# Kernel tuning notes

Measured on AMD Instinct MI355X. Metric: run time of the kernel, lower is better.

## Reference

```python
import jax, jax.numpy as jnp
import numpy as np

N, D, H, DPE, WALK, L, E = 2048, 512, 8, 16, 8, 3, 32768
HD = D // H
DFF = 4 * D


def setup_inputs() -> dict:
    key = jax.random.key(0)
    ks = jax.random.split(key, 16)
    s = 0.02
    return {
        "node_features": jax.random.normal(ks[0], (N, D), jnp.float32),
        "edge_index": jax.random.randint(ks[1], (2, E), 0, N, dtype=jnp.int32),
        "pe_proj_W": jax.random.normal(ks[2], (WALK, DPE), jnp.float32) * s,
        "pe_proj_b": jnp.zeros((DPE,), jnp.float32),
        "qkv_W": jax.random.normal(ks[3], (L, D, 3 * D), jnp.float32) * s,
        "qkv_b": jnp.zeros((L, 3 * D), jnp.float32),
        "peb_W": jax.random.normal(ks[4], (L, DPE, H), jnp.float32) * s,
        "peb_b": jnp.zeros((L, H), jnp.float32),
        "out_W": jax.random.normal(ks[5], (L, D, D), jnp.float32) * s,
        "out_b": jnp.zeros((L, D), jnp.float32),
        "ffn_W1": jax.random.normal(ks[6], (L, D, DFF), jnp.float32) * s,
        "ffn_b1": jnp.zeros((L, DFF), jnp.float32),
        "ffn_W2": jax.random.normal(ks[7], (L, DFF, D), jnp.float32) * s,
        "ffn_b2": jnp.zeros((L, D), jnp.float32),
        "ln1_g": jnp.ones((L, D), jnp.float32),
        "ln1_b": jnp.zeros((L, D), jnp.float32),
        "ln2_g": jnp.ones((L, D), jnp.float32),
        "ln2_b": jnp.zeros((L, D), jnp.float32),
    }


def _layer_norm(x, g, b, eps=1e-5):
    mu = x.mean(-1, keepdims=True)
    var = ((x - mu) ** 2).mean(-1, keepdims=True)
    return (x - mu) * jax.lax.rsqrt(var + eps) * g + b


def _rw_pe(edge_index, pe_proj_W, pe_proj_b, dtype):
    src, tgt = edge_index[0], edge_index[1]
    adj = jnp.zeros((N, N), dtype).at[src, tgt].set(1.0).at[tgt, src].set(1.0)
    deg = jnp.maximum(adj.sum(axis=1, keepdims=True), 1.0)
    T = adj / deg  # row-stochastic transition matrix

    def step(Tk, _):
        return Tk @ T, jnp.diagonal(Tk)

    _, diags = jax.lax.scan(step, T, None, length=WALK)  # [WALK, N]
    rw = diags.T  # [N, WALK] k-step return probabilities
    return rw @ pe_proj_W + pe_proj_b  # [N, DPE]


def reference(node_features, edge_index, pe_proj_W, pe_proj_b, qkv_W, qkv_b,
              peb_W, peb_b, out_W, out_b, ffn_W1, ffn_b1, ffn_W2, ffn_b2,
              ln1_g, ln1_b, ln2_g, ln2_b):
    pe = _rw_pe(edge_index, pe_proj_W, pe_proj_b, node_features.dtype)
    scale = HD ** -0.5
    x = node_features
    for l in range(L):
        qkv = (x @ qkv_W[l] + qkv_b[l]).reshape(N, 3, H, HD)
        q = jnp.transpose(qkv[:, 0], (1, 0, 2))  # [H, N, HD]
        k = jnp.transpose(qkv[:, 1], (1, 0, 2))
        v = jnp.transpose(qkv[:, 2], (1, 0, 2))
        pe_p = pe @ peb_W[l] + peb_b[l]  # [N, H]
        # bias[h, i, j] = pe_p[i, h] - pe_p[j, h]
        bias = pe_p.T[:, :, None] - pe_p.T[:, None, :]
        scores = jnp.einsum('hnd,hmd->hnm', q, k) * scale + bias
        attn = jax.nn.softmax(scores, axis=-1)
        o = jnp.einsum('hnm,hmd->hnd', attn, v)
        o = jnp.transpose(o, (1, 0, 2)).reshape(N, D) @ out_W[l] + out_b[l]
        x = _layer_norm(x + o, ln1_g[l], ln1_b[l])
        h = jax.nn.gelu(x @ ffn_W1[l] + ffn_b1[l], approximate=False)
        h = h @ ffn_W2[l] + ffn_b2[l]
        x = _layer_norm(x + h, ln2_g[l], ln2_b[l])
    return x
```

## Files before the change

### kernel.cpp

```cpp
#include <hip/hip_runtime.h>
#include <cstdint>
#include <cstddef>

#define NN 2048
#define DM 512
#define NH 8
#define HD 64
#define NL 3
#define DFFV 2048
#define NE 32768

typedef unsigned short u16;
typedef unsigned int u32;
typedef __attribute__((ext_vector_type(8))) short short8;
typedef __attribute__((ext_vector_type(4))) float float4v;

__device__ __forceinline__ float bf2f(u16 s){
  union { unsigned u; float f; } v; v.u = ((unsigned)s) << 16; return v.f;
}
__device__ __forceinline__ u16 f2bf(float f){
  union { float f; unsigned u; } v; v.f = f;
  unsigned r = v.u + 0x7fffu + ((v.u >> 16) & 1u);
  return (u16)(r >> 16);
}
__device__ __forceinline__ u16 f2bf_fast(float f){
  union { float f; unsigned u; } v; v.f = f;
  return (u16)((v.u + 0x8000u) >> 16);
}
__device__ __forceinline__ void gl_lds16(const void* g, void* l){
  __builtin_amdgcn_global_load_lds((const __attribute__((address_space(1))) void*)g,
                                   (__attribute__((address_space(3))) void*)l, 16, 0, 0);
}

__global__ void adj_scatter(const int* __restrict__ ei, float* __restrict__ A){
  int e = blockIdx.x*256 + threadIdx.x;
  if (e < NE){
    int s = ei[e], t = ei[NE + e];
    A[(size_t)s*NN + t] = 1.f;
    A[(size_t)t*NN + s] = 1.f;
  }
}

__global__ __launch_bounds__(256)
void rowsum_dinv(const float* __restrict__ A, float* __restrict__ dinv){
  int row = blockIdx.x, tid = threadIdx.x;
  __shared__ float red[4];
  float s = 0.f;
  for (int j=tid;j<NN;j+=256) s += A[(size_t)row*NN + j];
  #pragma unroll
  for (int off=32;off>0;off>>=1) s += __shfl_down(s, off);
  if ((tid&63)==0) red[tid>>6] = s;
  __syncthreads();
  if (tid==0) dinv[row] = rsqrtf(fmaxf(red[0]+red[1]+red[2]+red[3], 1.f));
}

__global__ void build_s(const float* __restrict__ A, const float* __restrict__ dinv,
                        u16* __restrict__ S){
  int j = blockIdx.x*256 + threadIdx.x;
  int i = blockIdx.y;
  float a = A[(size_t)i*NN + j];
  S[(size_t)i*NN + j] = f2bf(a * dinv[i] * dinv[j]);
}

__global__ __launch_bounds__(256)
void extract_nz(const u16* __restrict__ S, u32* __restrict__ nz, int* __restrict__ cnt){
  const int j = blockIdx.x, tid = threadIdx.x;
  __shared__ int lc;
  if (tid==0) lc = 0;
  __syncthreads();
  for (int c=tid; c<NN; c+=256){
    u16 v = S[(size_t)j*NN + c];
    if (v){
      int s = atomicAdd(&lc, 1);
      if (s < 128) nz[j*128 + s] = ((u32)c << 16) | v;
    }
  }
  __syncthreads();
  if (tid==0) cnt[j] = lc < 128 ? lc : 128;
}

__global__ __launch_bounds__(256)
void spmm(const u16* __restrict__ Bold, const u32* __restrict__ nz,
          const int* __restrict__ cnt, u16* __restrict__ Bnew)
{
  const int j = blockIdx.x, tid = threadIdx.x;
  __shared__ u32 lnz[128];
  __shared__ int lcnt;
  if (tid==0) lcnt = cnt[j];
  if (tid<128) lnz[tid] = nz[j*128 + tid];
  __syncthreads();
  const int n = lcnt;
  float acc[8] = {0,0,0,0,0,0,0,0};
  for (int e=0; e<n; e++){
    u32 p = lnz[e];
    int k = p >> 16;
    float wv = bf2f((u16)(p & 0xffffu));
    short8 rv = *(const short8*)&Bold[(size_t)k*NN + tid*8];
    #pragma unroll
    for (int t=0;t<8;t++) acc[t] = fmaf(bf2f((u16)rv[t]), wv, acc[t]);
  }
  short8 o;
  #pragma unroll
  for (int t=0;t<8;t++) o[t] = (short)f2bf(acc[t]);
  *(short8*)&Bnew[(size_t)j*NN + tid*8] = o;
}

__global__ __launch_bounds__(256)
void diag_pe(const u16* __restrict__ S, const u16* __restrict__ S2,
             const u16* __restrict__ S3, const u16* __restrict__ S4,
             const float* __restrict__ peW, const float* __restrict__ peb,
             float* __restrict__ pe)
{
  const int i = blockIdx.x, tid = threadIdx.x;
  float d[7] = {0,0,0,0,0,0,0};
  for (int j=tid;j<NN;j+=256){
    float s1 = bf2f(S [(size_t)i*NN + j]);
    float s2 = bf2f(S2[(size_t)i*NN + j]);
    float s3 = bf2f(S3[(size_t)i*NN + j]);
    float s4 = bf2f(S4[(size_t)i*NN + j]);
    d[0] += s1*s1; d[1] += s1*s2; d[2] += s2*s2; d[3] += s2*s3;
    d[4] += s3*s3; d[5] += s3*s4; d[6] += s4*s4;
  }
  __shared__ float red[28];
  #pragma unroll
  for (int t=0;t<7;t++){
    float v = d[t];
    #pragma unroll
    for (int off=32;off>0;off>>=1) v += __shfl_down(v, off);
    if ((tid&63)==0) red[t*4 + (tid>>6)] = v;
  }
  __syncthreads();
  if (tid < 16){
    float rr[8];
    rr[0] = bf2f(S[(size_t)i*NN + i]);
    #pragma unroll
    for (int t=0;t<7;t++) rr[t+1] = red[t*4]+red[t*4+1]+red[t*4+2]+red[t*4+3];
    float a = peb[tid];
    #pragma unroll
    for (int k=0;k<8;k++) a += rr[k]*peW[k*16 + tid];
    pe[(size_t)i*16 + tid] = a;
  }
}

__global__ void pe_proj2(const float* __restrict__ pe, const float* __restrict__ pebW,
                         const float* __restrict__ pebb, float* __restrict__ pebT){
  int n = blockIdx.x*256 + threadIdx.x;
  float pv[16];
  #pragma unroll
  for (int p=0;p<16;p++) pv[p] = pe[(size_t)n*16+p];
  for (int l=0;l<NL;l++)
    for (int h=0;h<NH;h++){
      float a = pebb[l*NH+h];
      #pragma unroll
      for (int p=0;p<16;p++) a += pv[p]*pebW[(l*16+p)*NH+h];
      pebT[((size_t)l*NH+h)*NN + n] = a;
    }
}

__global__ void init_x(const float* __restrict__ nf, float* __restrict__ x, u16* __restrict__ xbf){
  size_t i = (size_t)blockIdx.x*256 + threadIdx.x;
  float v = nf[i]; x[i] = v; xbf[i] = f2bf(v);
}

__global__ void transpose_w(const float* __restrict__ W, u16* __restrict__ WT, int K, int N){
  __shared__ float t[32][33];
  int l = blockIdx.z;
  W  += (size_t)l*K*N;
  WT += (size_t)l*K*N;
  int n0 = blockIdx.x*32, k0 = blockIdx.y*32;
  int tx = threadIdx.x, ty = threadIdx.y;
  #pragma unroll
  for (int i=0;i<32;i+=8) t[ty+i][tx] = W[(size_t)(k0+ty+i)*N + n0+tx];
  __syncthreads();
  #pragma unroll
  for (int i=0;i<32;i+=8) WT[(size_t)(n0+ty+i)*K + k0+tx] = f2bf(t[tx][ty+i]);
}

__global__ void pack_vt(const u16* __restrict__ qkv, u16* __restrict__ vT){
  __shared__ u16 t[32][33];
  int h = blockIdx.z, n0 = blockIdx.x*32, d0 = blockIdx.y*32;
  int tx = threadIdx.x, ty = threadIdx.y;
  #pragma unroll
  for (int i=0;i<32;i+=8) t[ty+i][tx] = qkv[(size_t)(n0+ty+i)*1536 + 1024 + h*64 + d0+tx];
  __syncthreads();
  #pragma unroll
  for (int i=0;i<32;i+=8) vT[(size_t)(h*64 + d0+ty+i)*NN + n0+tx] = t[tx][ty+i];
}

__global__ __launch_bounds__(256)
void ln_kernel(const float* __restrict__ xin, const float* __restrict__ add, int nsl,
               const float* __restrict__ g, const float* __restrict__ b,
               float* __restrict__ xout, u16* __restrict__ xbf)
{
  const int row = blockIdx.x, tid = threadIdx.x;
  __shared__ float red[8];
  const size_t base = (size_t)row*DM;
  float v0 = xin[base+tid];
  float v1 = xin[base+256+tid];
  for (int s=0;s<nsl;s++){
    v0 += add[(size_t)s*NN*DM + base+tid];
    v1 += add[(size_t)s*NN*DM + base+256+tid];
  }
  float s = v0+v1, sq = v0*v0 + v1*v1;
  #pragma unroll
  for (int off=32; off>0; off>>=1){ s += __shfl_down(s, off); sq += __shfl_down(sq, off); }
  if ((tid&63)==0){ red[tid>>6] = s; red[4+(tid>>6)] = sq; }
  __syncthreads();
  float mean = (red[0]+red[1]+red[2]+red[3]) * (1.f/512.f);
  float var  = (red[4]+red[5]+red[6]+red[7]) * (1.f/512.f) - mean*mean;
  float rstd = rsqrtf(var + 1e-5f);
  float y0 = (v0-mean)*rstd*g[tid]     + b[tid];
  float y1 = (v1-mean)*rstd*g[256+tid] + b[256+tid];
  xout[base+tid] = y0;     xout[base+256+tid] = y1;
  xbf[base+tid]  = f2bf(y0); xbf[base+256+tid] = f2bf(y1);
}

template<int OUTMODE, int GELU, int BIAS>
__global__ __launch_bounds__(256)
void gemm64(const u16* __restrict__ A, const u16* __restrict__ BT,
            const float* __restrict__ bias, void* __restrict__ Cout,
            int M, int N, int K, int ldc, int kper)
{
  __shared__ u16 As[64*32];
  __shared__ u16 Bs[64*32];
  const int tid = threadIdx.x, lane = tid & 63, wave = tid >> 6;
  const int q = lane >> 4, lo = lane & 15;
  const int bm = blockIdx.y, bn = blockIdx.x;
  const int wm = wave >> 1, wn = wave & 1;
  const int k_begin = blockIdx.z * kper, k_end = k_begin + kper;
  const int lrow  = lane >> 2;
  const int lkoff = (lane & 3) * 8;

  const u16* Ag = A  + ((size_t)bm*64 + 16*wave + lrow) * (size_t)K;
  const u16* Bg = BT + ((size_t)bn*64 + 16*wave + lrow) * (size_t)K;
  u16* AsW = As + (16*wave)*32;
  u16* BsW = Bs + (16*wave)*32;

  float4v acc[2][2] = {};

  for (int k0 = k_begin; k0 < k_end; k0 += 32){
    __syncthreads();
    gl_lds16(Ag + k0 + lkoff, AsW);
    gl_lds16(Bg + k0 + lkoff, BsW);
    __syncthreads();
    const short8* Ar = (const short8*)As;
    const short8* Br = (const short8*)Bs;
    short8 af[2], bfr[2];
    #pragma unroll
    for (int mt=0;mt<2;mt++) af[mt]  = Ar[(32*wm + 16*mt + lo)*4 + q];
    #pragma unroll
    for (int nt=0;nt<2;nt++) bfr[nt] = Br[(32*wn + 16*nt + lo)*4 + q];
    #pragma unroll
    for (int mt=0;mt<2;mt++)
      #pragma unroll
      for (int nt=0;nt<2;nt++)
        acc[mt][nt] = __builtin_amdgcn_mfma_f32_16x16x32_bf16(af[mt], bfr[nt], acc[mt][nt], 0, 0, 0);
  }

  float* Cf = (float*)Cout;
  u16*   Cb = (u16*)Cout;
  const size_t zoff = (OUTMODE == 2) ? (size_t)blockIdx.z * M * ldc : 0;
  #pragma unroll
  for (int mt=0;mt<2;mt++){
    const int row = bm*64 + 32*wm + 16*mt + q*4;
    #pragma unroll
    for (int nt=0;nt<2;nt++){
      const int col = bn*64 + 32*wn + 16*nt + lo;
      float bb = BIAS ? bias[col] : 0.f;
      #pragma unroll
      for (int r=0;r<4;r++){
        float v = acc[mt][nt][r];
        if (OUTMODE == 2){
          if (BIAS && blockIdx.z == 0) v += bb;
          Cf[zoff + (size_t)(row+r)*ldc + col] = v;
        } else {
          v += bb;
          if (GELU) v = 0.5f*v*(1.f + erff(v*0.70710678118654752f));
          if (OUTMODE == 1) Cb[(size_t)(row+r)*ldc + col] = f2bf(v);
          else              Cf[(size_t)(row+r)*ldc + col] = v;
        }
      }
    }
  }
}

__global__ __launch_bounds__(256)
void attn_part(const u16* __restrict__ qkv, const u16* __restrict__ vT,
               const float* __restrict__ pebT, float* __restrict__ Opart,
               float* __restrict__ Lsum)
{
  __shared__ u16 Ks[64*72];
  __shared__ u16 Vs[64*72];
  __shared__ u16 Ps[64*72];
  __shared__ float CB[64];
  const int tid = threadIdx.x, lane = tid&63, wave = tid>>6;
  const int q = lane>>4, lo = lane&15;
  const int qb = blockIdx.x, h = blockIdx.y, ks = blockIdx.z;
  const int i0 = qb*64;
  const int part = (ks*NH + h)*32 + qb;

  short8 qf[2];
  #pragma unroll
  for (int kk=0;kk<2;kk++)
    qf[kk] = *(const short8*)&qkv[(size_t)(i0 + 16*wave + lo)*1536 + h*64 + kk*32 + q*8];

  float l_r[4] = {0.f,0.f,0.f,0.f};
  float4v o_acc[4] = {};

  const int j_begin = ks*512, j_end = j_begin + 512;
  for (int j0 = j_begin; j0 < j_end; j0 += 64){
    __syncthreads();
    for (int c = tid; c < 512; c += 256){
      int row = c >> 3, off = c & 7;
      *(float4v*)&Ks[row*72 + off*8] =
        *(const float4v*)&qkv[(size_t)(j0+row)*1536 + 512 + h*64 + off*8];
      *(float4v*)&Vs[row*72 + off*8] =
        *(const float4v*)&vT[(size_t)(h*64+row)*NN + j0 + off*8];
    }
    if (tid < 64) CB[tid] = pebT[(size_t)h*NN + j0 + tid] * 1.4426950408889634f;
    __syncthreads();

    float4v sacc[4] = {};
    const short8* Kr = (const short8*)Ks;
    #pragma unroll
    for (int kk=0; kk<2; kk++){
      #pragma unroll
      for (int nt=0; nt<4; nt++){
        short8 bfr = Kr[(16*nt + lo)*9 + kk*4 + q];
        sacc[nt] = __builtin_amdgcn_mfma_f32_16x16x32_bf16(qf[kk], bfr, sacc[nt], 0,0,0);
      }
    }
    #pragma unroll
    for (int nt=0; nt<4; nt++){
      float cb = CB[16*nt + lo];
      #pragma unroll
      for (int r=0;r<4;r++){
        float p = exp2f(fmaf(sacc[nt][r], 0.180336880f, -cb));
        l_r[r] += p;
        Ps[(16*wave + q*4 + r)*72 + 16*nt + lo] = f2bf_fast(p);
      }
    }
    const short8* Pr = (const short8*)Ps;
    const short8* Vr = (const short8*)Vs;
    #pragma unroll
    for (int kk=0;kk<2;kk++){
      short8 af = Pr[(16*wave + lo)*9 + kk*4 + q];
      #pragma unroll
      for (int nt=0;nt<4;nt++){
        short8 bfr = Vr[(16*nt + lo)*9 + kk*4 + q];
        o_acc[nt] = __builtin_amdgcn_mfma_f32_16x16x32_bf16(af, bfr, o_acc[nt], 0,0,0);
      }
    }
  }
  #pragma unroll
  for (int r=0;r<4;r++){
    float s = l_r[r];
    s += __shfl_xor(s, 1);
    s += __shfl_xor(s, 2);
    s += __shfl_xor(s, 4);
    s += __shfl_xor(s, 8);
    l_r[r] = s;
  }
  float* Op = Opart + (size_t)part*4096;
  #pragma unroll
  for (int nt=0;nt<4;nt++){
    #pragma unroll
    for (int r=0;r<4;r++)
      Op[(16*wave + q*4 + r)*64 + 16*nt + lo] = o_acc[nt][r];
  }
  if (lo == 0){
    #pragma unroll
    for (int r=0;r<4;r++)
      Lsum[part*64 + 16*wave + q*4 + r] = l_r[r];
  }
}

__global__ __launch_bounds__(256)
void attn_combine(const float* __restrict__ Opart, const float* __restrict__ Lsum,
                  u16* __restrict__ obuf)
{
  const int qb = blockIdx.x, h = blockIdx.y, tid = threadIdx.x;
  __shared__ float invL[64];
  if (tid < 64){
    float L = 0.f;
    #pragma unroll
    for (int k=0;k<4;k++) L += Lsum[((k*NH + h)*32 + qb)*64 + tid];
    invL[tid] = 1.f / L;
  }
  __syncthreads();
  const int col = tid & 63, r0 = (tid >> 6) * 16;
  #pragma unroll
  for (int r=0;r<16;r++){
    int row = r0 + r;
    float acc = 0.f;
    #pragma unroll
    for (int k=0;k<4;k++)
      acc += Opart[((size_t)((k*NH + h)*32 + qb))*4096 + row*64 + col];
    obuf[(size_t)(qb*64 + row)*DM + h*64 + col] = f2bf(acc * invL[row]);
  }
}

extern "C" void kernel_launch(void* const* d_in, const int* in_sizes, int n_in,
                              void* d_out, int out_size, void* d_ws, size_t ws_size,
                              hipStream_t stream) {
  const float* nf   = (const float*)d_in[0];
  const int*   ei   = (const int*)d_in[1];
  const float* peW  = (const float*)d_in[2];
  const float* peb  = (const float*)d_in[3];
  const float* qkvW = (const float*)d_in[4];
  const float* qkvb = (const float*)d_in[5];
  const float* pebW = (const float*)d_in[6];
  const float* pebb = (const float*)d_in[7];
  const float* outW = (const float*)d_in[8];
  const float* outb = (const float*)d_in[9];
  const float* f1W  = (const float*)d_in[10];
  const float* f1b  = (const float*)d_in[11];
  const float* f2W  = (const float*)d_in[12];
  const float* f2b  = (const float*)d_in[13];
  const float* ln1g = (const float*)d_in[14];
  const float* ln1b = (const float*)d_in[15];
  const float* ln2g = (const float*)d_in[16];
  const float* ln2b = (const float*)d_in[17];
  (void)in_sizes; (void)n_in; (void)out_size; (void)ws_size;

  char* w = (char*)d_ws;
  constexpr size_t OFF_A     = 0;
  constexpr size_t OFF_S     = OFF_A + 16777216;
  constexpr size_t OFF_S2    = OFF_S + 8388608;
  constexpr size_t OFF_S3    = OFF_S2 + 8388608;
  constexpr size_t OFF_S4    = OFF_S3 + 8388608;
  constexpr size_t OFF_DINV  = OFF_S4 + 8388608;
  constexpr size_t OFF_PE    = OFF_DINV + 8192;
  constexpr size_t OFF_PEBT  = OFF_PE + 131072;
  constexpr size_t OFF_QKVT  = OFF_PEBT + 196608;
  constexpr size_t OFF_OUTT  = OFF_QKVT + 4718592;
  constexpr size_t OFF_F1T   = OFF_OUTT + 1572864;
  constexpr size_t OFF_F2T   = OFF_F1T + 6291456;
  constexpr size_t OFF_X     = OFF_F2T + 6291456;
  constexpr size_t OFF_XBF   = OFF_X + 4194304;
  constexpr size_t OFF_QKVB  = OFF_XBF + 2097152;
  constexpr size_t OFF_VT    = OFF_QKVB + 6291456;
  constexpr size_t OFF_OBUF  = OFF_VT + 2097152;
  constexpr size_t OFF_NZ    = OFF_OBUF + 2097152;
  constexpr size_t OFF_CNT   = OFF_NZ + 1048576;
  constexpr size_t OFF_ML    = OFF_CNT + 8192;
  constexpr size_t OFF_HBUF  = OFF_ML + 524288;

  float* A     = (float*)(w + OFF_A);
  u16*   S     = (u16*)  (w + OFF_S);
  u16*   S2    = (u16*)  (w + OFF_S2);
  u16*   S3    = (u16*)  (w + OFF_S3);
  u16*   S4    = (u16*)  (w + OFF_S4);
  float* dinv  = (float*)(w + OFF_DINV);
  float* pe    = (float*)(w + OFF_PE);
  float* pebT  = (float*)(w + OFF_PEBT);
  u16*   qkvT  = (u16*)  (w + OFF_QKVT);
  u16*   outT  = (u16*)  (w + OFF_OUTT);
  u16*   f1T   = (u16*)  (w + OFF_F1T);
  u16*   f2T   = (u16*)  (w + OFF_F2T);
  float* x     = (float*)(w + OFF_X);
  u16*   xbf   = (u16*)  (w + OFF_XBF);
  u16*   qkvB  = (u16*)  (w + OFF_QKVB);
  u16*   vT    = (u16*)  (w + OFF_VT);
  u16*   obuf  = (u16*)  (w + OFF_OBUF);
  u32*   NZ    = (u32*)  (w + OFF_NZ);
  int*   CNT   = (int*)  (w + OFF_CNT);
  float* Lsum  = (float*)(w + OFF_ML);
  u16*   hbuf  = (u16*)  (w + OFF_HBUF);
  float* Opart = A;

  hipMemsetAsync(A, 0, 16777216, stream);
  adj_scatter<<<dim3(NE/256), 256, 0, stream>>>(ei, A);
  rowsum_dinv<<<dim3(NN), 256, 0, stream>>>(A, dinv);
  build_s<<<dim3(NN/256, NN), 256, 0, stream>>>(A, dinv, S);
  extract_nz<<<dim3(NN), 256, 0, stream>>>(S, NZ, CNT);
  spmm<<<dim3(NN), 256, 0, stream>>>(S,  NZ, CNT, S2);
  spmm<<<dim3(NN), 256, 0, stream>>>(S2, NZ, CNT, S3);
  spmm<<<dim3(NN), 256, 0, stream>>>(S3, NZ, CNT, S4);
  diag_pe<<<dim3(NN), 256, 0, stream>>>(S, S2, S3, S4, peW, peb, pe);
  pe_proj2<<<dim3(NN/256), 256, 0, stream>>>(pe, pebW, pebb, pebT);

  transpose_w<<<dim3(1536/32, 512/32, NL), dim3(32,8), 0, stream>>>(qkvW, qkvT, 512, 1536);
  transpose_w<<<dim3(512/32,  512/32, NL), dim3(32,8), 0, stream>>>(outW, outT, 512, 512);
  transpose_w<<<dim3(2048/32, 512/32, NL), dim3(32,8), 0, stream>>>(f1W,  f1T,  512, 2048);
  transpose_w<<<dim3(512/32, 2048/32, NL), dim3(32,8), 0, stream>>>(f2W,  f2T,  2048, 512);
  init_x<<<dim3(NN*DM/256), 256, 0, stream>>>(nf, x, xbf);

  for (int l = 0; l < NL; l++){
    gemm64<1,0,1><<<dim3(24,32,1), 256, 0, stream>>>(
        xbf, qkvT + (size_t)l*1536*512, qkvb + l*1536, qkvB, 2048, 1536, 512, 1536, 512);
    pack_vt<<<dim3(64,2,8), dim3(32,8), 0, stream>>>(qkvB, vT);
    attn_part<<<dim3(32,8,4), 256, 0, stream>>>(qkvB, vT, pebT + (size_t)l*NH*NN, Opart, Lsum);
    attn_combine<<<dim3(32,8), 256, 0, stream>>>(Opart, Lsum, obuf);

    gemm64<2,0,1><<<dim3(8,32,2), 256, 0, stream>>>(
        obuf, outT + (size_t)l*512*512, outb + l*512, A, 2048, 512, 512, 512, 256);
    ln_kernel<<<dim3(NN), 256, 0, stream>>>(x, A, 2, ln1g + l*512, ln1b + l*512, x, xbf);

    gemm64<1,1,1><<<dim3(32,32,1), 256, 0, stream>>>(
        xbf, f1T + (size_t)l*2048*512, f1b + l*2048, hbuf, 2048, 2048, 512, 2048, 512);
    gemm64<2,0,1><<<dim3(8,32,4), 256, 0, stream>>>(
        hbuf, f2T + (size_t)l*512*2048, f2b + l*512, A, 2048, 512, 2048, 512, 512);
    ln_kernel<<<dim3(NN), 256, 0, stream>>>(x, A, 4, ln2g + l*512, ln2b + l*512, x, xbf);
  }

  hipMemcpyAsync(d_out, x, (size_t)NN*DM*4, hipMemcpyDeviceToDevice, stream);
}
```

Baseline: 513.4 us.

## Fuse preprocessing kernels, compute V transposed via GEMM, enlarge attention query tiles

Merges build_s with nonzero extraction, folds the per-layer PE bias projection into diag_pe, and merges the four weight transposes into one launch. This cuts launch count and extra passes over the 2048x2048 matrices. V^T is now produced directly by a swapped-operand GEMM with a row-bias mode, which removes the pack_vt kernel. Attention processes 128 query rows per block so each K/V tile is reused more. The final layer norm writes straight to the output, which removes the trailing memcpy. The costs are fewer attention blocks (512 instead of 1024) and more register pressure.

```diff
diff --git a/kernel.cpp b/kernel.cpp
--- a/kernel.cpp
+++ b/kernel.cpp
@@ -7,7 +7,6 @@
 #define NH 8
 #define HD 64
 #define NL 3
-#define DFFV 2048
 #define NE 32768
 
 typedef unsigned short u16;
@@ -54,29 +53,25 @@
   if (tid==0) dinv[row] = rsqrtf(fmaxf(red[0]+red[1]+red[2]+red[3], 1.f));
 }
 
-__global__ void build_s(const float* __restrict__ A, const float* __restrict__ dinv,
-                        u16* __restrict__ S){
-  int j = blockIdx.x*256 + threadIdx.x;
-  int i = blockIdx.y;
-  float a = A[(size_t)i*NN + j];
-  S[(size_t)i*NN + j] = f2bf(a * dinv[i] * dinv[j]);
-}
-
-__global__ __launch_bounds__(256)
-void extract_nz(const u16* __restrict__ S, u32* __restrict__ nz, int* __restrict__ cnt){
-  const int j = blockIdx.x, tid = threadIdx.x;
+__global__ __launch_bounds__(256)
+void build_s_nz(const float* __restrict__ A, const float* __restrict__ dinv,
+                u16* __restrict__ S, u32* __restrict__ nz, int* __restrict__ cnt){
+  const int i = blockIdx.x, tid = threadIdx.x;
   __shared__ int lc;
   if (tid==0) lc = 0;
   __syncthreads();
-  for (int c=tid; c<NN; c+=256){
-    u16 v = S[(size_t)j*NN + c];
+  const float di = dinv[i];
+  for (int j=tid; j<NN; j+=256){
+    float a = A[(size_t)i*NN + j];
+    u16 v = f2bf(a * di * dinv[j]);
+    S[(size_t)i*NN + j] = v;
     if (v){
       int s = atomicAdd(&lc, 1);
-      if (s < 128) nz[j*128 + s] = ((u32)c << 16) | v;
-    }
-  }
-  __syncthreads();
-  if (tid==0) cnt[j] = lc < 128 ? lc : 128;
+      if (s < 128) nz[i*128 + s] = ((u32)j << 16) | v;
+    }
+  }
+  __syncthreads();
+  if (tid==0) cnt[i] = lc < 128 ? lc : 128;
 }
 
 __global__ __launch_bounds__(256)
@@ -109,7 +104,8 @@
 void diag_pe(const u16* __restrict__ S, const u16* __restrict__ S2,
              const u16* __restrict__ S3, const u16* __restrict__ S4,
              const float* __restrict__ peW, const float* __restrict__ peb,
-             float* __restrict__ pe)
+             const float* __restrict__ pebW, const float* __restrict__ pebb,
+             float* __restrict__ pebT)
 {
   const int i = blockIdx.x, tid = threadIdx.x;
   float d[7] = {0,0,0,0,0,0,0};
@@ -122,6 +118,7 @@
     d[4] += s3*s3; d[5] += s3*s4; d[6] += s4*s4;
   }
   __shared__ float red[28];
+  __shared__ float pv[16];
   #pragma unroll
   for (int t=0;t<7;t++){
     float v = d[t];
@@ -138,23 +135,16 @@
     float a = peb[tid];
     #pragma unroll
     for (int k=0;k<8;k++) a += rr[k]*peW[k*16 + tid];
-    pe[(size_t)i*16 + tid] = a;
-  }
-}
-
-__global__ void pe_proj2(const float* __restrict__ pe, const float* __restrict__ pebW,
-                         const float* __restrict__ pebb, float* __restrict__ pebT){
-  int n = blockIdx.x*256 + threadIdx.x;
-  float pv[16];
-  #pragma unroll
-  for (int p=0;p<16;p++) pv[p] = pe[(size_t)n*16+p];
-  for (int l=0;l<NL;l++)
-    for (int h=0;h<NH;h++){
-      float a = pebb[l*NH+h];
-      #pragma unroll
-      for (int p=0;p<16;p++) a += pv[p]*pebW[(l*16+p)*NH+h];
-      pebT[((size_t)l*NH+h)*NN + n] = a;
-    }
+    pv[tid] = a;
+  }
+  __syncthreads();
+  if (tid < 24){
+    int l = tid >> 3, h = tid & 7;
+    float a = pebb[l*NH + h];
+    #pragma unroll
+    for (int p=0;p<16;p++) a += pv[p]*pebW[(l*16+p)*NH + h];
+    pebT[((size_t)l*NH + h)*NN + i] = a;
+  }
 }
 
 __global__ void init_x(const float* __restrict__ nf, float* __restrict__ x, u16* __restrict__ xbf){
@@ -162,29 +152,29 @@
   float v = nf[i]; x[i] = v; xbf[i] = f2bf(v);
 }
 
-__global__ void transpose_w(const float* __restrict__ W, u16* __restrict__ WT, int K, int N){
+__global__ __launch_bounds__(256)
+void transpose_all(const float* __restrict__ qkvW, const float* __restrict__ outW,
+                   const float* __restrict__ f1W,  const float* __restrict__ f2W,
+                   u16* __restrict__ qkvT, u16* __restrict__ outT,
+                   u16* __restrict__ f1T,  u16* __restrict__ f2T)
+{
   __shared__ float t[32][33];
-  int l = blockIdx.z;
+  int gid = blockIdx.x;
+  int l = gid / 3072, r = gid % 3072;
+  const float* W; u16* WT; int K, N, bx, by;
+  if (r < 768)      { W=qkvW; WT=qkvT; K=512;  N=1536; bx=r%48;        by=r/48; }
+  else if (r < 1024){ int u=r-768;  W=outW; WT=outT; K=512;  N=512;  bx=u%16; by=u/16; }
+  else if (r < 2048){ int u=r-1024; W=f1W;  WT=f1T;  K=512;  N=2048; bx=u%64; by=u/64; }
+  else              { int u=r-2048; W=f2W;  WT=f2T;  K=2048; N=512;  bx=u%16; by=u/16; }
   W  += (size_t)l*K*N;
   WT += (size_t)l*K*N;
-  int n0 = blockIdx.x*32, k0 = blockIdx.y*32;
-  int tx = threadIdx.x, ty = threadIdx.y;
+  int n0 = bx*32, k0 = by*32;
+  int tx = threadIdx.x & 31, ty = threadIdx.x >> 5;
   #pragma unroll
   for (int i=0;i<32;i+=8) t[ty+i][tx] = W[(size_t)(k0+ty+i)*N + n0+tx];
   __syncthreads();
   #pragma unroll
   for (int i=0;i<32;i+=8) WT[(size_t)(n0+ty+i)*K + k0+tx] = f2bf(t[tx][ty+i]);
-}
-
-__global__ void pack_vt(const u16* __restrict__ qkv, u16* __restrict__ vT){
-  __shared__ u16 t[32][33];
-  int h = blockIdx.z, n0 = blockIdx.x*32, d0 = blockIdx.y*32;
-  int tx = threadIdx.x, ty = threadIdx.y;
-  #pragma unroll
-  for (int i=0;i<32;i+=8) t[ty+i][tx] = qkv[(size_t)(n0+ty+i)*1536 + 1024 + h*64 + d0+tx];
-  __syncthreads();
-  #pragma unroll
-  for (int i=0;i<32;i+=8) vT[(size_t)(h*64 + d0+ty+i)*NN + n0+tx] = t[tx][ty+i];
 }
 
 __global__ __launch_bounds__(256)
@@ -266,10 +256,11 @@
     #pragma unroll
     for (int nt=0;nt<2;nt++){
       const int col = bn*64 + 32*wn + 16*nt + lo;
-      float bb = BIAS ? bias[col] : 0.f;
+      float bbc = (BIAS==1) ? bias[col] : 0.f;
       #pragma unroll
       for (int r=0;r<4;r++){
         float v = acc[mt][nt][r];
+        float bb = (BIAS==2) ? bias[row+r] : bbc;
         if (OUTMODE == 2){
           if (BIAS && blockIdx.z == 0) v += bb;
           Cf[zoff + (size_t)(row+r)*ldc + col] = v;
@@ -285,27 +276,29 @@
 }
 
 __global__ __launch_bounds__(256)
-void attn_part(const u16* __restrict__ qkv, const u16* __restrict__ vT,
+void attn_part(const u16* __restrict__ qkB, const u16* __restrict__ vT,
                const float* __restrict__ pebT, float* __restrict__ Opart,
                float* __restrict__ Lsum)
 {
   __shared__ u16 Ks[64*72];
   __shared__ u16 Vs[64*72];
-  __shared__ u16 Ps[64*72];
+  __shared__ u16 Ps[128*72];
   __shared__ float CB[64];
   const int tid = threadIdx.x, lane = tid&63, wave = tid>>6;
   const int q = lane>>4, lo = lane&15;
   const int qb = blockIdx.x, h = blockIdx.y, ks = blockIdx.z;
-  const int i0 = qb*64;
-  const int part = (ks*NH + h)*32 + qb;
-
-  short8 qf[2];
-  #pragma unroll
-  for (int kk=0;kk<2;kk++)
-    qf[kk] = *(const short8*)&qkv[(size_t)(i0 + 16*wave + lo)*1536 + h*64 + kk*32 + q*8];
-
-  float l_r[4] = {0.f,0.f,0.f,0.f};
-  float4v o_acc[4] = {};
+  const int i0 = qb*128;
+  const int part = (ks*NH + h)*16 + qb;
+
+  short8 qf[2][2];
+  #pragma unroll
+  for (int mt=0;mt<2;mt++)
+    #pragma unroll
+    for (int kk=0;kk<2;kk++)
+      qf[kk][mt] = *(const short8*)&qkB[(size_t)(i0 + 32*wave + 16*mt + lo)*1024 + h*64 + kk*32 + q*8];
+
+  float l_r[2][4] = {};
+  float4v o_acc[2][4] = {};
 
   const int j_begin = ks*512, j_end = j_begin + 512;
   for (int j0 = j_begin; j0 < j_end; j0 += 64){
@@ -313,65 +306,69 @@
     for (int c = tid; c < 512; c += 256){
       int row = c >> 3, off = c & 7;
       *(float4v*)&Ks[row*72 + off*8] =
-        *(const float4v*)&qkv[(size_t)(j0+row)*1536 + 512 + h*64 + off*8];
+        *(const float4v*)&qkB[(size_t)(j0+row)*1024 + 512 + h*64 + off*8];
       *(float4v*)&Vs[row*72 + off*8] =
         *(const float4v*)&vT[(size_t)(h*64+row)*NN + j0 + off*8];
     }
     if (tid < 64) CB[tid] = pebT[(size_t)h*NN + j0 + tid] * 1.4426950408889634f;
     __syncthreads();
 
-    float4v sacc[4] = {};
+    float4v sacc[2][4] = {};
     const short8* Kr = (const short8*)Ks;
     #pragma unroll
     for (int kk=0; kk<2; kk++){
       #pragma unroll
       for (int nt=0; nt<4; nt++){
         short8 bfr = Kr[(16*nt + lo)*9 + kk*4 + q];
-        sacc[nt] = __builtin_amdgcn_mfma_f32_16x16x32_bf16(qf[kk], bfr, sacc[nt], 0,0,0);
+        #pragma unroll
+        for (int mt=0; mt<2; mt++)
+          sacc[mt][nt] = __builtin_amdgcn_mfma_f32_16x16x32_bf16(qf[kk][mt], bfr, sacc[mt][nt], 0,0,0);
       }
     }
     #pragma unroll
-    for (int nt=0; nt<4; nt++){
-      float cb = CB[16*nt + lo];
-      #pragma unroll
-      for (int r=0;r<4;r++){
-        float p = exp2f(fmaf(sacc[nt][r], 0.180336880f, -cb));
-        l_r[r] += p;
-        Ps[(16*wave + q*4 + r)*72 + 16*nt + lo] = f2bf_fast(p);
+    for (int mt=0; mt<2; mt++)
+      #pragma unroll
+      for (int nt=0; nt<4; nt++){
+        float cb = CB[16*nt + lo];
+        #pragma unroll
+        for (int r=0;r<4;r++){
+          float p = exp2f(fmaf(sacc[mt][nt][r], 0.180336880f, -cb));
+          l_r[mt][r] += p;
+          Ps[(32*wave + 16*mt + q*4 + r)*72 + 16*nt + lo] = f2bf_fast(p);
+        }
       }
-    }
     const short8* Pr = (const short8*)Ps;
     const short8* Vr = (const short8*)Vs;
     #pragma unroll
     for (int kk=0;kk<2;kk++){
-      short8 af = Pr[(16*wave + lo)*9 + kk*4 + q];
-      #pragma unroll
-      for (int nt=0;nt<4;nt++){
-        short8 bfr = Vr[(16*nt + lo)*9 + kk*4 + q];
-        o_acc[nt] = __builtin_amdgcn_mfma_f32_16x16x32_bf16(af, bfr, o_acc[nt], 0,0,0);
+      #pragma unroll
+      for (int mt=0;mt<2;mt++){
+        short8 af = Pr[(32*wave + 16*mt + lo)*9 + kk*4 + q];
+        #pragma unroll
+        for (int nt=0;nt<4;nt++){
+          short8 bfr = Vr[(16*nt + lo)*9 + kk*4 + q];
+          o_acc[mt][nt] = __builtin_amdgcn_mfma_f32_16x16x32_bf16(af, bfr, o_acc[mt][nt], 0,0,0);
+        }
       }
     }
   }
-  #pragma unroll
-  for (int r=0;r<4;r++){
-    float s = l_r[r];
-    s += __shfl_xor(s, 1);
-    s += __shfl_xor(s, 2);
-    s += __shfl_xor(s, 4);
-    s += __shfl_xor(s, 8);
-    l_r[r] = s;
-  }
-  float* Op = Opart + (size_t)part*4096;
-  #pragma unroll
-  for (int nt=0;nt<4;nt++){
-    #pragma unroll
-    for (int r=0;r<4;r++)
-      Op[(16*wave + q*4 + r)*64 + 16*nt + lo] = o_acc[nt][r];
-  }
-  if (lo == 0){
-    #pragma unroll
-    for (int r=0;r<4;r++)
-      Lsum[part*64 + 16*wave + q*4 + r] = l_r[r];
+  float* Op = Opart + (size_t)part*8192;
+  #pragma unroll
+  for (int mt=0;mt<2;mt++){
+    #pragma unroll
+    for (int r=0;r<4;r++){
+      float s = l_r[mt][r];
+      s += __shfl_xor(s, 1);
+      s += __shfl_xor(s, 2);
+      s += __shfl_xor(s, 4);
+      s += __shfl_xor(s, 8);
+      if (lo == 0) Lsum[part*128 + 32*wave + 16*mt + q*4 + r] = s;
+    }
+    #pragma unroll
+    for (int nt=0;nt<4;nt++)
+      #pragma unroll
+      for (int r=0;r<4;r++)
+        Op[(32*wave + 16*mt + q*4 + r)*64 + 16*nt + lo] = o_acc[mt][nt][r];
   }
 }
 
@@ -380,23 +377,23 @@
                   u16* __restrict__ obuf)
 {
   const int qb = blockIdx.x, h = blockIdx.y, tid = threadIdx.x;
-  __shared__ float invL[64];
-  if (tid < 64){
+  __shared__ float invL[128];
+  if (tid < 128){
     float L = 0.f;
     #pragma unroll
-    for (int k=0;k<4;k++) L += Lsum[((k*NH + h)*32 + qb)*64 + tid];
+    for (int k=0;k<4;k++) L += Lsum[((k*NH + h)*16 + qb)*128 + tid];
     invL[tid] = 1.f / L;
   }
   __syncthreads();
-  const int col = tid & 63, r0 = (tid >> 6) * 16;
-  #pragma unroll
-  for (int r=0;r<16;r++){
+  const int col = tid & 63, r0 = (tid >> 6) * 32;
+  #pragma unroll
+  for (int r=0;r<32;r++){
     int row = r0 + r;
     float acc = 0.f;
     #pragma unroll
     for (int k=0;k<4;k++)
-      acc += Opart[((size_t)((k*NH + h)*32 + qb))*4096 + row*64 + col];
-    obuf[(size_t)(qb*64 + row)*DM + h*64 + col] = f2bf(acc * invL[row]);
+      acc += Opart[((size_t)((k*NH + h)*16 + qb))*8192 + row*64 + col];
+    obuf[(size_t)(qb*128 + row)*DM + h*64 + col] = f2bf(acc * invL[row]);
   }
 }
 
@@ -430,21 +427,20 @@
   constexpr size_t OFF_S3    = OFF_S2 + 8388608;
   constexpr size_t OFF_S4    = OFF_S3 + 8388608;
   constexpr size_t OFF_DINV  = OFF_S4 + 8388608;
-  constexpr size_t OFF_PE    = OFF_DINV + 8192;
-  constexpr size_t OFF_PEBT  = OFF_PE + 131072;
+  constexpr size_t OFF_PEBT  = OFF_DINV + 8192;
   constexpr size_t OFF_QKVT  = OFF_PEBT + 196608;
   constexpr size_t OFF_OUTT  = OFF_QKVT + 4718592;
   constexpr size_t OFF_F1T   = OFF_OUTT + 1572864;
   constexpr size_t OFF_F2T   = OFF_F1T + 6291456;
   constexpr size_t OFF_X     = OFF_F2T + 6291456;
   constexpr size_t OFF_XBF   = OFF_X + 4194304;
-  constexpr size_t OFF_QKVB  = OFF_XBF + 2097152;
-  constexpr size_t OFF_VT    = OFF_QKVB + 6291456;
+  constexpr size_t OFF_QKB   = OFF_XBF + 2097152;
+  constexpr size_t OFF_VT    = OFF_QKB + 4194304;
   constexpr size_t OFF_OBUF  = OFF_VT + 2097152;
   constexpr size_t OFF_NZ    = OFF_OBUF + 2097152;
   constexpr size_t OFF_CNT   = OFF_NZ + 1048576;
-  constexpr size_t OFF_ML    = OFF_CNT + 8192;
-  constexpr size_t OFF_HBUF  = OFF_ML + 524288;
+  constexpr size_t OFF_LS    = OFF_CNT + 8192;
+  constexpr size_t OFF_HBUF  = OFF_LS + 262144;
 
   float* A     = (float*)(w + OFF_A);
   u16*   S     = (u16*)  (w + OFF_S);
@@ -452,7 +448,6 @@
   u16*   S3    = (u16*)  (w + OFF_S3);
   u16*   S4    = (u16*)  (w + OFF_S4);
   float* dinv  = (float*)(w + OFF_DINV);
-  float* pe    = (float*)(w + OFF_PE);
   float* pebT  = (float*)(w + OFF_PEBT);
   u16*   qkvT  = (u16*)  (w + OFF_QKVT);
   u16*   outT  = (u16*)  (w + OFF_OUTT);
@@ -460,38 +455,35 @@
   u16*   f2T   = (u16*)  (w + OFF_F2T);
   float* x     = (float*)(w + OFF_X);
   u16*   xbf   = (u16*)  (w + OFF_XBF);
-  u16*   qkvB  = (u16*)  (w + OFF_QKVB);
+  u16*   qkB   = (u16*)  (w + OFF_QKB);
   u16*   vT    = (u16*)  (w + OFF_VT);
   u16*   obuf  = (u16*)  (w + OFF_OBUF);
   u32*   NZ    = (u32*)  (w + OFF_NZ);
   int*   CNT   = (int*)  (w + OFF_CNT);
-  float* Lsum  = (float*)(w + OFF_ML);
+  float* Lsum  = (float*)(w + OFF_LS);
   u16*   hbuf  = (u16*)  (w + OFF_HBUF);
   float* Opart = A;
 
   hipMemsetAsync(A, 0, 16777216, stream);
   adj_scatter<<<dim3(NE/256), 256, 0, stream>>>(ei, A);
   rowsum_dinv<<<dim3(NN), 256, 0, stream>>>(A, dinv);
-  build_s<<<dim3(NN/256, NN), 256, 0, stream>>>(A, dinv, S);
-  extract_nz<<<dim3(NN), 256, 0, stream>>>(S, NZ, CNT);
+  build_s_nz<<<dim3(NN), 256, 0, stream>>>(A, dinv, S, NZ, CNT);
   spmm<<<dim3(NN), 256, 0, stream>>>(S,  NZ, CNT, S2);
   spmm<<<dim3(NN), 256, 0, stream>>>(S2, NZ, CNT, S3);
   spmm<<<dim3(NN), 256, 0, stream>>>(S3, NZ, CNT, S4);
-  diag_pe<<<dim3(NN), 256, 0, stream>>>(S, S2, S3, S4, peW, peb, pe);
-  pe_proj2<<<dim3(NN/256), 256, 0, stream>>>(pe, pebW, pebb, pebT);
-
-  transpose_w<<<dim3(1536/32, 512/32, NL), dim3(32,8), 0, stream>>>(qkvW, qkvT, 512, 1536);
-  transpose_w<<<dim3(512/32,  512/32, NL), dim3(32,8), 0, stream>>>(outW, outT, 512, 512);
-  transpose_w<<<dim3(2048/32, 512/32, NL), dim3(32,8), 0, stream>>>(f1W,  f1T,  512, 2048);
-  transpose_w<<<dim3(512/32, 2048/32, NL), dim3(32,8), 0, stream>>>(f2W,  f2T,  2048, 512);
+  diag_pe<<<dim3(NN), 256, 0, stream>>>(S, S2, S3, S4, peW, peb, pebW, pebb, pebT);
+
+  transpose_all<<<dim3(9216), 256, 0, stream>>>(qkvW, outW, f1W, f2W, qkvT, outT, f1T, f2T);
   init_x<<<dim3(NN*DM/256), 256, 0, stream>>>(nf, x, xbf);
 
   for (int l = 0; l < NL; l++){
-    gemm64<1,0,1><<<dim3(24,32,1), 256, 0, stream>>>(
-        xbf, qkvT + (size_t)l*1536*512, qkvb + l*1536, qkvB, 2048, 1536, 512, 1536, 512);
-    pack_vt<<<dim3(64,2,8), dim3(32,8), 0, stream>>>(qkvB, vT);
-    attn_part<<<dim3(32,8,4), 256, 0, stream>>>(qkvB, vT, pebT + (size_t)l*NH*NN, Opart, Lsum);
-    attn_combine<<<dim3(32,8), 256, 0, stream>>>(Opart, Lsum, obuf);
+    gemm64<1,0,1><<<dim3(16,32,1), 256, 0, stream>>>(
+        xbf, qkvT + (size_t)l*1536*512, qkvb + l*1536, qkB, 2048, 1024, 512, 1024, 512);
+    gemm64<1,0,2><<<dim3(32,8,1), 256, 0, stream>>>(
+        qkvT + (size_t)l*1536*512 + (size_t)1024*512, xbf, qkvb + l*1536 + 1024, vT,
+        512, 2048, 512, 2048, 512);
+    attn_part<<<dim3(16,8,4), 256, 0, stream>>>(qkB, vT, pebT + (size_t)l*NH*NN, Opart, Lsum);
+    attn_combine<<<dim3(16,8), 256, 0, stream>>>(Opart, Lsum, obuf);
 
     gemm64<2,0,1><<<dim3(8,32,2), 256, 0, stream>>>(
         obuf, outT + (size_t)l*512*512, outb + l*512, A, 2048, 512, 512, 512, 256);
@@ -501,8 +493,7 @@
         xbf, f1T + (size_t)l*2048*512, f1b + l*2048, hbuf, 2048, 2048, 512, 2048, 512);
     gemm64<2,0,1><<<dim3(8,32,4), 256, 0, stream>>>(
         hbuf, f2T + (size_t)l*512*2048, f2b + l*512, A, 2048, 512, 2048, 512, 512);
-    ln_kernel<<<dim3(NN), 256, 0, stream>>>(x, A, 4, ln2g + l*512, ln2b + l*512, x, xbf);
-  }
-
-  hipMemcpyAsync(d_out, x, (size_t)NN*DM*4, hipMemcpyDeviceToDevice, stream);
-}
+    float* xout = (l == NL-1) ? (float*)d_out : x;
+    ln_kernel<<<dim3(NN), 256, 0, stream>>>(x, A, 4, ln2g + l*512, ln2b + l*512, xout, xbf);
+  }
+}
```

New measurement: 511.7 us. About the same (-0.3%).
